# Performance work log

Measured on AMD Instinct MI355X. Metric: run time of the kernel, lower is better.

Reference implementation:

```python
import jax, jax.numpy as jnp
import numpy as np

C = 128
Y_ANCHORS = 16
X_ANCHORS = 16
H = 256
W = 256


def _cubic(t):
    # PyTorch bicubic convolution kernel, a = -0.75
    a = -0.75
    at = jnp.abs(t)
    near = ((a + 2.0) * at - (a + 3.0)) * at * at + 1.0
    far = (((at - 5.0) * at + 8.0) * at - 4.0) * a
    return jnp.where(at <= 1.0, near, jnp.where(at < 2.0, far, 0.0))


def _bicubic_weight_matrix(out_size, in_size):
    # Row-stochastic (out_size, in_size) matrix replicating torch
    # F.interpolate(mode='bicubic', align_corners=False) with index clamping.
    scale = in_size / out_size
    src = (jnp.arange(out_size, dtype=jnp.float32) + 0.5) * scale - 0.5
    i0 = jnp.floor(src)
    t = src - i0
    offs = jnp.arange(-1, 3)
    w = _cubic(t[:, None] - offs[None, :].astype(jnp.float32))  # (out, 4)
    idx = jnp.clip(i0[:, None].astype(jnp.int32) + offs[None, :], 0, in_size - 1)
    Wm = jnp.zeros((out_size, in_size), jnp.float32)
    return Wm.at[jnp.arange(out_size)[:, None], idx].add(w)


def setup_inputs() -> dict:
    key = jax.random.key(0)
    k1, k2, k3 = jax.random.split(key, 3)
    x = jax.random.normal(k1, (2, C, H, W), jnp.float32)
    mean_table = jax.random.normal(k2, (Y_ANCHORS, X_ANCHORS, C), jnp.float32)
    # stds from previously processed tiles are positive; shift rand away from 0
    std_table = jax.random.uniform(k3, (Y_ANCHORS, X_ANCHORS, C), jnp.float32) + 0.5
    weight = jnp.ones((1, C, 1, 1), jnp.float32)
    bias = jnp.zeros((1, C, 1, 1), jnp.float32)
    return {
        'x': x, 'mean_table': mean_table, 'std_table': std_table,
        'weight': weight, 'bias': bias,
        'y_anchor': 4, 'x_anchor': 5, 'pre_y1_anchor': 5, 'pre_x1_anchor': 6,
    }


def reference(x, mean_table, std_table, weight, bias,
              y_anchor, x_anchor, pre_y1_anchor, pre_x1_anchor):
    real_x, pre_x = jnp.split(x, 2, axis=0)  # each (1,C,H,W)
    h, w = real_x.shape[2], real_x.shape[3]
    n = h * w

    # --- prefetched tile: unbiased instance-norm stats, written into the tables
    pre_mean = jnp.mean(pre_x, axis=(2, 3))  # (1,C)
    pre_var = jnp.sum((pre_x - pre_mean[:, :, None, None]) ** 2, axis=(2, 3)) / (n - 1)
    pre_std = jnp.sqrt(pre_var)  # (1,C), torch.std_mean default unbiased
    mean_table = mean_table.at[pre_y1_anchor, pre_x1_anchor].set(pre_mean[0])
    std_table = std_table.at[pre_y1_anchor, pre_x1_anchor].set(pre_std[0])

    # --- replication pad (left=1,right=2,top=1,bottom=2) -> (Y+3, X+3, C)
    pm = jnp.pad(mean_table, ((1, 2), (1, 2), (0, 0)), mode='edge')
    ps = jnp.pad(std_table, ((1, 2), (1, 2), (0, 0)), mode='edge')

    # --- 4x4 anchor window around the current tile
    mean_patch = jax.lax.dynamic_slice(pm, (y_anchor, x_anchor, 0), (4, 4, C))
    std_patch = jax.lax.dynamic_slice(ps, (y_anchor, x_anchor, 0), (4, 4, C))

    # --- bicubic 4x4 -> (3h,3w), center-crop to (h,w); crop folded into weights
    Wy = _bicubic_weight_matrix(3 * h, 4)[h // 2:h // 2 + h]  # (h,4)
    Wx = _bicubic_weight_matrix(3 * w, 4)[w // 2:w // 2 + w]  # (w,4)
    mean_map = jnp.einsum('oy,yxc,px->cop', Wy, mean_patch, Wx)[None]        # (1,C,h,w)
    stdinv_map = jnp.einsum('oy,yxc,px->cop', Wy, 1.0 / std_patch, Wx)[None]  # (1,C,h,w)

    real = (real_x - mean_map) * stdinv_map * weight + bias
    pre = (pre_x - pre_mean[:, :, None, None]) / pre_std[:, :, None, None] * weight + bias
    return jnp.concatenate([real, pre], axis=0)
```

## Files before the change

### kernel.cpp

```cpp
#include <hip/hip_runtime.h>
#include <hip/hip_bf16.h>

#define C 128
#define H 256
#define W 256
#define HW (H * W)
#define CHW (C * H * W)
#define NTAB 16

__device__ __forceinline__ float cubic075(float u) {
    float au = fabsf(u);
    float near_ = (1.25f * au - 2.25f) * au * au + 1.0f;
    float far_  = -0.75f * (((au - 5.0f) * au + 8.0f) * au - 4.0f);
    return au <= 1.0f ? near_ : (au < 2.0f ? far_ : 0.0f);
}

__device__ __forceinline__ void bicubic_w4(int o, float* w4) {
    const float scale = 4.0f / 768.0f;
    float src = ((float)(o + 128) + 0.5f) * scale - 0.5f;
    float i0f = floorf(src);
    float t = src - i0f;
    int i0 = (int)i0f;
    w4[0] = w4[1] = w4[2] = w4[3] = 0.0f;
#pragma unroll
    for (int j = 0; j < 4; ++j) {
        int off = j - 1;
        float wv = cubic075(t - (float)off);
        int idx = i0 + off;
        idx = idx < 0 ? 0 : (idx > 3 ? 3 : idx);
        w4[idx] += wv;
    }
}

__global__ __launch_bounds__(256) void stats_kernel(const float* __restrict__ x,
                                                    float* __restrict__ ws) {
    int c = blockIdx.x >> 3;
    int seg = blockIdx.x & 7;
    const float4* x4 = (const float4*)(x + CHW) + (size_t)c * (HW / 4) + seg * 2048;
    float s = 0.0f, s2 = 0.0f;
#pragma unroll
    for (int k = 0; k < 8; ++k) {
        float4 v = x4[k * 256 + threadIdx.x];
        s  += v.x + v.y + v.z + v.w;
        s2 += v.x * v.x + v.y * v.y + v.z * v.z + v.w * v.w;
    }
#pragma unroll
    for (int off = 32; off > 0; off >>= 1) {
        s  += __shfl_down(s, off);
        s2 += __shfl_down(s2, off);
    }
    __shared__ float sd[8];
    int wid = threadIdx.x >> 6;
    if ((threadIdx.x & 63) == 0) { sd[wid] = s; sd[4 + wid] = s2; }
    __syncthreads();
    if (threadIdx.x == 0) {
        ws[c * 8 + seg]        = sd[0] + sd[1] + sd[2] + sd[3];
        ws[1024 + c * 8 + seg] = sd[4] + sd[5] + sd[6] + sd[7];
    }
}

__device__ __forceinline__ void channel_stats(const float* __restrict__ ws, int c,
                                              float& mean, float& stdv) {
    float s = 0.0f, s2 = 0.0f;
#pragma unroll
    for (int k = 0; k < 8; ++k) { s += ws[c * 8 + k]; s2 += ws[1024 + c * 8 + k]; }
    const float n = (float)HW;
    mean = s / n;
    float var = (s2 - s * s / n) / (n - 1.0f);
    stdv = sqrtf(var);
}

__global__ __launch_bounds__(256) void main_kernel(
    const float* __restrict__ x,
    const float* __restrict__ mean_table, const float* __restrict__ std_table,
    const float* __restrict__ weight, const float* __restrict__ bias,
    const int* __restrict__ yA, const int* __restrict__ xA,
    const int* __restrict__ pyA, const int* __restrict__ pxA,
    const float* __restrict__ ws, float* __restrict__ out) {
    int b = blockIdx.x;
    int t = threadIdx.x;
    if (b < 1024) {
        int o = b & 255;
        int g = b >> 8;
        __shared__ float patchM[16 * 32];
        __shared__ float patchI[16 * 32];
        __shared__ float Am[4 * 32], Ai[4 * 32], Wgt[32], Bs[32];
        {
            int cc = t & 31;
            int e0 = t >> 5;
            int c = g * 32 + cc;
            float mean, stdv;
            channel_stats(ws, c, mean, stdv);
            int ya = min(max(*yA, 0), 15);
            int xa = min(max(*xA, 0), 15);
            int py = *pyA, px = *pxA;
#pragma unroll
            for (int e = e0; e < 16; e += 8) {
                int row = min(max(ya + (e >> 2) - 1, 0), NTAB - 1);
                int col = min(max(xa + (e & 3) - 1, 0), NTAB - 1);
                float m, s;
                if (row == py && col == px) { m = mean; s = stdv; }
                else {
                    m = mean_table[(row * NTAB + col) * C + c];
                    s = std_table[(row * NTAB + col) * C + c];
                }
                patchM[e * 32 + cc] = m;
                patchI[e * 32 + cc] = 1.0f / s;
            }
            if (e0 == 0) { Wgt[cc] = weight[c]; Bs[cc] = bias[c]; }
        }
        __syncthreads();
        float wy[4];
        bicubic_w4(o, wy);
        {
            int xx = (t >> 5) & 3;
            int cc = t & 31;
            const float* src = (t < 128) ? patchM : patchI;
            float a = 0.0f;
#pragma unroll
            for (int y = 0; y < 4; ++y) a += wy[y] * src[(y * 4 + xx) * 32 + cc];
            if (t < 128) Am[xx * 32 + cc] = a;
            else         Ai[xx * 32 + cc] = a;
        }
        __syncthreads();

        int w = t >> 6, l = t & 63;
        float wx[4][4];
#pragma unroll
        for (int e = 0; e < 4; ++e) bicubic_w4(4 * l + e, wx[e]);
        const float4* xin = (const float4*)x;
        float4* outp = (float4*)out;
#pragma unroll
        for (int k = 0; k < 8; ++k) {
            int cc = w * 8 + k;
            int c = g * 32 + cc;
            size_t base = ((size_t)c * HW + o * W) / 4 + l;
            float4 v = xin[base];
            float wgt = Wgt[cc], bsv = Bs[cc];
            float r[4], vv[4] = {v.x, v.y, v.z, v.w};
#pragma unroll
            for (int e = 0; e < 4; ++e) {
                float m = 0.0f, iv = 0.0f;
#pragma unroll
                for (int xx = 0; xx < 4; ++xx) {
                    m  += wx[e][xx] * Am[xx * 32 + cc];
                    iv += wx[e][xx] * Ai[xx * 32 + cc];
                }
                r[e] = (vv[e] - m) * iv * wgt + bsv;
            }
            float4 ro = {r[0], r[1], r[2], r[3]};
            outp[base] = ro;
        }
    } else {
        int bb = b - 1024;
        __shared__ float Sp[C], Bp[C];
        if (t < C) {
            float mean, stdv;
            channel_stats(ws, t, mean, stdv);
            float sp = weight[t] / stdv;
            Sp[t] = sp;
            Bp[t] = bias[t] - mean * sp;
        }
        __syncthreads();
        const float4* xin = (const float4*)(x + CHW);
        float4* outp = (float4*)(out + CHW);
        int i = bb * 256 + t;
#pragma unroll
        for (int k = 0; k < 8; ++k) {
            int j = i + k * 262144;
            float4 v = xin[j];
            int c = j >> 14;
            float sp = Sp[c], bp = Bp[c];
            float4 r;
            r.x = v.x * sp + bp;
            r.y = v.y * sp + bp;
            r.z = v.z * sp + bp;
            r.w = v.w * sp + bp;
            outp[j] = r;
        }
    }
}

extern "C" void kernel_launch(void* const* d_in, const int* in_sizes, int n_in,
                              void* d_out, int out_size, void* d_ws, size_t ws_size,
                              hipStream_t stream) {
    const float* x          = (const float*)d_in[0];
    const float* mean_table = (const float*)d_in[1];
    const float* std_table  = (const float*)d_in[2];
    const float* weight     = (const float*)d_in[3];
    const float* bias       = (const float*)d_in[4];
    const int* yA  = (const int*)d_in[5];
    const int* xA  = (const int*)d_in[6];
    const int* pyA = (const int*)d_in[7];
    const int* pxA = (const int*)d_in[8];
    float* out = (float*)d_out;
    float* ws  = (float*)d_ws;

    stats_kernel<<<C * 8, 256, 0, stream>>>(x, ws);
    main_kernel<<<2048, 256, 0, stream>>>(x, mean_table, std_table, weight, bias,
                                          yA, xA, pyA, pxA, ws, out);
}
```

Measured before the change: 136.4 us.

## Fuse stats and normalization into one cooperative kernel with register-held prefetch tile

Replaces the two-kernel sequence with a single cooperative launch of 1024 blocks. Each block reads its slice of the prefetched tile, reduces partial sums, waits on a grid-wide sync, and then normalizes those values from registers, so the second read of that half of the input goes away. After that the block runs the bicubic-interpolated normalization for the real tile. It also caches the Am/Ai coefficients in registers. The cost is a grid barrier, a residency requirement of four blocks per CU, and higher register pressure. If the cooperative launch fails, it falls back to the old two kernels.

```diff
diff --git a/kernel.cpp b/kernel.cpp
--- a/kernel.cpp
+++ b/kernel.cpp
@@ -1,5 +1,7 @@
 #include <hip/hip_runtime.h>
-#include <hip/hip_bf16.h>
+#include <hip/hip_cooperative_groups.h>
+
+namespace cg = cooperative_groups;
 
 #define C 128
 #define H 256
@@ -32,6 +34,151 @@
     }
 }
 
+__device__ __forceinline__ void channel_stats(const float* __restrict__ ws, int c,
+                                              float& mean, float& stdv) {
+    float s = 0.0f, s2 = 0.0f;
+#pragma unroll
+    for (int k = 0; k < 8; ++k) { s += ws[c * 8 + k]; s2 += ws[1024 + c * 8 + k]; }
+    const float n = (float)HW;
+    mean = s / n;
+    float var = (s2 - s * s / n) / (n - 1.0f);
+    stdv = sqrtf(var);
+}
+
+__global__ __launch_bounds__(256, 4) void fused_kernel(
+    const float* __restrict__ x,
+    const float* __restrict__ mean_table, const float* __restrict__ std_table,
+    const float* __restrict__ weight, const float* __restrict__ bias,
+    const int* __restrict__ yA, const int* __restrict__ xA,
+    const int* __restrict__ pyA, const int* __restrict__ pxA,
+    float* __restrict__ ws, float* __restrict__ out) {
+    int b = blockIdx.x;
+    int t = threadIdx.x;
+
+    const float4* pre4 = (const float4*)(x + CHW);
+    size_t base1 = (size_t)b * 2048 + t;
+    float4 v[8];
+    float s = 0.0f, s2 = 0.0f;
+#pragma unroll
+    for (int k = 0; k < 8; ++k) {
+        float4 vv = pre4[base1 + k * 256];
+        v[k] = vv;
+        s  += vv.x + vv.y + vv.z + vv.w;
+        s2 += vv.x * vv.x + vv.y * vv.y + vv.z * vv.z + vv.w * vv.w;
+    }
+#pragma unroll
+    for (int off = 32; off > 0; off >>= 1) {
+        s  += __shfl_down(s, off);
+        s2 += __shfl_down(s2, off);
+    }
+    __shared__ float sd[8];
+    int wid = t >> 6;
+    if ((t & 63) == 0) { sd[wid] = s; sd[4 + wid] = s2; }
+    __syncthreads();
+    if (t == 0) {
+        ws[b]        = sd[0] + sd[1] + sd[2] + sd[3];
+        ws[1024 + b] = sd[4] + sd[5] + sd[6] + sd[7];
+    }
+    __threadfence();
+    cg::this_grid().sync();
+    __threadfence();
+
+    {
+        int c = b >> 3;
+        float mean, stdv;
+        channel_stats(ws, c, mean, stdv);
+        float sp = weight[c] / stdv;
+        float bp = bias[c] - mean * sp;
+        float4* outp = (float4*)(out + CHW);
+#pragma unroll
+        for (int k = 0; k < 8; ++k) {
+            float4 r;
+            r.x = v[k].x * sp + bp;
+            r.y = v[k].y * sp + bp;
+            r.z = v[k].z * sp + bp;
+            r.w = v[k].w * sp + bp;
+            outp[base1 + k * 256] = r;
+        }
+    }
+
+    {
+        int o = b & 255;
+        int g = b >> 8;
+        __shared__ float patchM[16 * 32];
+        __shared__ float patchI[16 * 32];
+        __shared__ float Am[4 * 32], Ai[4 * 32], Wgt[32], Bs[32];
+        {
+            int cc = t & 31;
+            int e0 = t >> 5;
+            int c = g * 32 + cc;
+            float mean, stdv;
+            channel_stats(ws, c, mean, stdv);
+            int ya = min(max(*yA, 0), 15);
+            int xa = min(max(*xA, 0), 15);
+            int py = *pyA, px = *pxA;
+#pragma unroll
+            for (int e = e0; e < 16; e += 8) {
+                int row = min(max(ya + (e >> 2) - 1, 0), NTAB - 1);
+                int col = min(max(xa + (e & 3) - 1, 0), NTAB - 1);
+                float m, sv;
+                if (row == py && col == px) { m = mean; sv = stdv; }
+                else {
+                    m  = mean_table[(row * NTAB + col) * C + c];
+                    sv = std_table[(row * NTAB + col) * C + c];
+                }
+                patchM[e * 32 + cc] = m;
+                patchI[e * 32 + cc] = 1.0f / sv;
+            }
+            if (e0 == 0) { Wgt[cc] = weight[c]; Bs[cc] = bias[c]; }
+        }
+        __syncthreads();
+        float wy[4];
+        bicubic_w4(o, wy);
+        {
+            int xx = (t >> 5) & 3;
+            int cc = t & 31;
+            const float* src = (t < 128) ? patchM : patchI;
+            float a = 0.0f;
+#pragma unroll
+            for (int y = 0; y < 4; ++y) a += wy[y] * src[(y * 4 + xx) * 32 + cc];
+            if (t < 128) Am[xx * 32 + cc] = a;
+            else         Ai[xx * 32 + cc] = a;
+        }
+        __syncthreads();
+
+        int w = t >> 6, l = t & 63;
+        float wx[4][4];
+#pragma unroll
+        for (int e = 0; e < 4; ++e) bicubic_w4(4 * l + e, wx[e]);
+        const float4* xin = (const float4*)x;
+        float4* outp = (float4*)out;
+#pragma unroll
+        for (int k = 0; k < 8; ++k) {
+            int cc = w * 8 + k;
+            int c = g * 32 + cc;
+            size_t base = ((size_t)c * HW + o * W) / 4 + l;
+            float4 v4 = xin[base];
+            float wgt = Wgt[cc], bsv = Bs[cc];
+            float am[4], ai[4];
+#pragma unroll
+            for (int q = 0; q < 4; ++q) { am[q] = Am[q * 32 + cc]; ai[q] = Ai[q * 32 + cc]; }
+            float r[4], vv[4] = {v4.x, v4.y, v4.z, v4.w};
+#pragma unroll
+            for (int e = 0; e < 4; ++e) {
+                float m = 0.0f, iv = 0.0f;
+#pragma unroll
+                for (int q = 0; q < 4; ++q) {
+                    m  += wx[e][q] * am[q];
+                    iv += wx[e][q] * ai[q];
+                }
+                r[e] = (vv[e] - m) * iv * wgt + bsv;
+            }
+            float4 ro = {r[0], r[1], r[2], r[3]};
+            outp[base] = ro;
+        }
+    }
+}
+
 __global__ __launch_bounds__(256) void stats_kernel(const float* __restrict__ x,
                                                     float* __restrict__ ws) {
     int c = blockIdx.x >> 3;
@@ -57,17 +204,6 @@
         ws[c * 8 + seg]        = sd[0] + sd[1] + sd[2] + sd[3];
         ws[1024 + c * 8 + seg] = sd[4] + sd[5] + sd[6] + sd[7];
     }
-}
-
-__device__ __forceinline__ void channel_stats(const float* __restrict__ ws, int c,
-                                              float& mean, float& stdv) {
-    float s = 0.0f, s2 = 0.0f;
-#pragma unroll
-    for (int k = 0; k < 8; ++k) { s += ws[c * 8 + k]; s2 += ws[1024 + c * 8 + k]; }
-    const float n = (float)HW;
-    mean = s / n;
-    float var = (s2 - s * s / n) / (n - 1.0f);
-    stdv = sqrtf(var);
 }
 
 __global__ __launch_bounds__(256) void main_kernel(
@@ -98,14 +234,14 @@
             for (int e = e0; e < 16; e += 8) {
                 int row = min(max(ya + (e >> 2) - 1, 0), NTAB - 1);
                 int col = min(max(xa + (e & 3) - 1, 0), NTAB - 1);
-                float m, s;
-                if (row == py && col == px) { m = mean; s = stdv; }
+                float m, sv;
+                if (row == py && col == px) { m = mean; sv = stdv; }
                 else {
-                    m = mean_table[(row * NTAB + col) * C + c];
-                    s = std_table[(row * NTAB + col) * C + c];
+                    m  = mean_table[(row * NTAB + col) * C + c];
+                    sv = std_table[(row * NTAB + col) * C + c];
                 }
                 patchM[e * 32 + cc] = m;
-                patchI[e * 32 + cc] = 1.0f / s;
+                patchI[e * 32 + cc] = 1.0f / sv;
             }
             if (e0 == 0) { Wgt[cc] = weight[c]; Bs[cc] = bias[c]; }
         }
@@ -135,16 +271,16 @@
             int cc = w * 8 + k;
             int c = g * 32 + cc;
             size_t base = ((size_t)c * HW + o * W) / 4 + l;
-            float4 v = xin[base];
+            float4 v4 = xin[base];
             float wgt = Wgt[cc], bsv = Bs[cc];
-            float r[4], vv[4] = {v.x, v.y, v.z, v.w};
+            float r[4], vv[4] = {v4.x, v4.y, v4.z, v4.w};
 #pragma unroll
             for (int e = 0; e < 4; ++e) {
                 float m = 0.0f, iv = 0.0f;
 #pragma unroll
-                for (int xx = 0; xx < 4; ++xx) {
-                    m  += wx[e][xx] * Am[xx * 32 + cc];
-                    iv += wx[e][xx] * Ai[xx * 32 + cc];
+                for (int q = 0; q < 4; ++q) {
+                    m  += wx[e][q] * Am[q * 32 + cc];
+                    iv += wx[e][q] * Ai[q * 32 + cc];
                 }
                 r[e] = (vv[e] - m) * iv * wgt + bsv;
             }
@@ -168,14 +304,14 @@
 #pragma unroll
         for (int k = 0; k < 8; ++k) {
             int j = i + k * 262144;
-            float4 v = xin[j];
+            float4 v4 = xin[j];
             int c = j >> 14;
             float sp = Sp[c], bp = Bp[c];
             float4 r;
-            r.x = v.x * sp + bp;
-            r.y = v.y * sp + bp;
-            r.z = v.z * sp + bp;
-            r.w = v.w * sp + bp;
+            r.x = v4.x * sp + bp;
+            r.y = v4.y * sp + bp;
+            r.z = v4.z * sp + bp;
+            r.w = v4.w * sp + bp;
             outp[j] = r;
         }
     }
@@ -196,7 +332,14 @@
     float* out = (float*)d_out;
     float* ws  = (float*)d_ws;
 
-    stats_kernel<<<C * 8, 256, 0, stream>>>(x, ws);
-    main_kernel<<<2048, 256, 0, stream>>>(x, mean_table, std_table, weight, bias,
-                                          yA, xA, pyA, pxA, ws, out);
-}
+    void* args[] = {(void*)&x, (void*)&mean_table, (void*)&std_table, (void*)&weight,
+                    (void*)&bias, (void*)&yA, (void*)&xA, (void*)&pyA, (void*)&pxA,
+                    (void*)&ws, (void*)&out};
+    hipError_t err = hipLaunchCooperativeKernel((void*)fused_kernel, dim3(1024),
+                                                dim3(256), args, 0, stream);
+    if (err != hipSuccess) {
+        stats_kernel<<<C * 8, 256, 0, stream>>>(x, ws);
+        main_kernel<<<2048, 256, 0, stream>>>(x, mean_table, std_table, weight, bias,
+                                              yA, xA, pyA, pxA, ws, out);
+    }
+}
```

After: 326.1 us. 139% more time.
